# Optimization experiments

Hardware: AMD Instinct MI355X
Metric: run time of the kernel (lower is better)

The kernel has to match this reference:

```python
import jax, jax.numpy as jnp
import numpy as np

G, P, DEG = 1024, 75, 8            # graphs, nodes per graph, out-degree
N, E = G * P, G * P * DEG
KS, DIM = 5, 2
K = KS ** DIM                      # 25 spline weight matrices
VOX = 4                            # 2x2 voxel grid per graph (size=14 over [0,27.99])


def setup_inputs():
    key = jax.random.key(0)
    ks = jax.random.split(key, 14)
    x = jax.random.uniform(ks[0], (N, 1), dtype=jnp.float32)            # pixel intensities
    src = jnp.repeat(jnp.arange(N, dtype=jnp.int32), DEG)
    dst = (src // P) * P + jax.random.randint(ks[1], (E,), 0, P, dtype=jnp.int32)
    edge_index = jnp.stack([src, dst])                                   # [2,E], within-graph edges
    edge_attr = jax.random.uniform(ks[2], (E, DIM), dtype=jnp.float32)  # Cartesian pseudo-coords in [0,1]
    batch = jnp.repeat(jnp.arange(G, dtype=jnp.int32), P)
    pos = jax.random.uniform(ks[3], (N, DIM), dtype=jnp.float32) * 27.99

    def nrm(k, shape, fan_in):
        return jax.random.normal(k, shape, jnp.float32) / np.float32(np.sqrt(fan_in))

    W1 = nrm(ks[4], (K, 1, 32), 1.0)
    root1 = nrm(ks[5], (1, 32), 1.0)
    b1 = jnp.zeros((32,), jnp.float32)
    W2 = nrm(ks[6], (K, 32, 64), 32.0)
    root2 = nrm(ks[7], (32, 64), 32.0)
    b2 = jnp.zeros((64,), jnp.float32)
    W3 = nrm(ks[8], (K, 64, 64), 64.0)
    root3 = nrm(ks[9], (64, 64), 64.0)
    b3 = jnp.zeros((64,), jnp.float32)
    fc1_w = nrm(ks[10], (4 * 64, 128), 256.0)
    fc1_b = jnp.zeros((128,), jnp.float32)
    fc2_w = nrm(ks[11], (128, 10), 128.0)
    fc2_b = jnp.zeros((10,), jnp.float32)
    return dict(x=x, edge_index=edge_index, edge_attr=edge_attr, batch=batch, pos=pos,
                W1=W1, root1=root1, b1=b1, W2=W2, root2=root2, b2=b2,
                W3=W3, root3=root3, b3=b3,
                fc1_w=fc1_w, fc1_b=fc1_b, fc2_w=fc2_w, fc2_b=fc2_b)


def spline_basis(u):
    """Degree-1 open B-spline basis, dim=2, kernel_size=5. u:[E,2] in [0,1].
    Returns basis [E,4] and flat weight indices [E,4]."""
    p = u * (KS - 1)
    lo = jnp.clip(jnp.floor(p), 0.0, KS - 1)
    frac = p - lo
    lo_i = lo.astype(jnp.int32)
    hi_i = jnp.minimum(lo_i + 1, KS - 1)
    w0 = jnp.stack([1.0 - frac[:, 0], frac[:, 0]], 1)   # [E,2]
    w1 = jnp.stack([1.0 - frac[:, 1], frac[:, 1]], 1)
    i0 = jnp.stack([lo_i[:, 0], hi_i[:, 0]], 1)
    i1 = jnp.stack([lo_i[:, 1], hi_i[:, 1]], 1)
    basis = (w0[:, :, None] * w1[:, None, :]).reshape(-1, 4)      # [E,4]
    idx = (i0[:, :, None] + KS * i1[:, None, :]).reshape(-1, 4)   # [E,4]
    return basis, idx


def spline_conv(h, src, dst, basis, idx, W, root, bias):
    # per-node transform under all K kernel weights: [N,K,O]
    y = jnp.einsum('ni,kio->nko', h, W)
    O = W.shape[2]
    msg = jnp.zeros((src.shape[0], O), h.dtype)
    for s in range(4):  # 4 B-spline corner contributions (fixed small loop)
        msg = msg + basis[:, s:s + 1] * y[src, idx[:, s]]
    agg = jax.ops.segment_sum(msg, dst, num_segments=N)
    deg = jax.ops.segment_sum(jnp.ones((src.shape[0],), h.dtype), dst, num_segments=N)
    agg = agg / jnp.maximum(deg, 1.0)[:, None]          # aggr='mean'
    return agg + h @ root + bias


def reference(x, edge_index, edge_attr, batch, pos,
              W1, root1, b1, W2, root2, b2, W3, root3, b3,
              fc1_w, fc1_b, fc2_w, fc2_b):
    src, dst = edge_index[0], edge_index[1]
    basis, idx = spline_basis(edge_attr)
    h = jax.nn.elu(spline_conv(x, src, dst, basis, idx, W1, root1, b1))
    h = jax.nn.elu(spline_conv(h, src, dst, basis, idx, W2, root2, b2))
    h = jax.nn.elu(spline_conv(h, src, dst, basis, idx, W3, root3, b3))
    # voxel_grid(size=14, start=0, end=27.99) -> 2x2 grid per graph
    vox = jnp.clip((pos / 14.0).astype(jnp.int32), 0, 1)          # [N,2]
    cluster = batch * VOX + vox[:, 0] + 2 * vox[:, 1]
    pooled = jax.ops.segment_max(h, cluster, num_segments=G * VOX)
    pooled = jnp.where(jnp.isneginf(pooled), 0.0, pooled)         # empty voxels -> 0
    graph_x = pooled.reshape(G, VOX * 64)                          # [G, 256]
    graph_x = jax.nn.elu(graph_x @ fc1_w + fc1_b)                  # dropout: eval mode (identity)
    logits = graph_x @ fc2_w + fc2_b
    return jax.nn.log_softmax(logits, axis=1)
```

## Files before the change

### kernel.cpp

```cpp
#include <hip/hip_runtime.h>
#include <math.h>

#define NG 1024
#define NP 75
#define NE_G 600
#define E_TOT 614400
#define NK 25
#define NSEG 1875
#define SST 104
#define YTST 104
#define HST 72

typedef _Float16 half8 __attribute__((ext_vector_type(8)));
typedef float floatx4 __attribute__((ext_vector_type(4)));

#define WS_WT2 0
#define WS_WT3 51200
#define WS_R2T 153600
#define WS_R3T 155648

__device__ __forceinline__ float elu_f(float x) {
    return x > 0.f ? x : (expf(x) - 1.f);
}
__device__ __forceinline__ float h16f(unsigned short b) {
    union { unsigned short u; _Float16 h; } c; c.u = b; return (float)c.h;
}
__device__ __forceinline__ _Float16 bits16(unsigned short b) {
    union { unsigned short u; _Float16 h; } c; c.u = b; return c.h;
}
__device__ __forceinline__ unsigned short f16bits(float v) {
    union { _Float16 h; unsigned short u; } c; c.h = (_Float16)v; return c.u;
}

__global__ void __launch_bounds__(256) prep_weights(
    const float* __restrict__ W2, const float* __restrict__ root2,
    const float* __restrict__ W3, const float* __restrict__ root3,
    _Float16* __restrict__ ws)
{
    int i = blockIdx.x * 256 + threadIdx.x;
    int stride = gridDim.x * 256;
    for (int t = i; t < 25 * 64 * 32; t += stride) {
        int k = t >> 11, o = (t >> 5) & 63, ci = t & 31;
        ws[WS_WT2 + t] = (_Float16)W2[(k * 32 + ci) * 64 + o];
    }
    for (int t = i; t < 25 * 64 * 64; t += stride) {
        int k = t >> 12, o = (t >> 6) & 63, ci = t & 63;
        ws[WS_WT3 + t] = (_Float16)W3[(k * 64 + ci) * 64 + o];
    }
    for (int t = i; t < 64 * 32; t += stride) {
        int o = t >> 5, ci = t & 31;
        ws[WS_R2T + t] = (_Float16)root2[ci * 64 + o];
    }
    for (int t = i; t < 64 * 64; t += stride) {
        int o = t >> 6, ci = t & 63;
        ws[WS_R3T + t] = (_Float16)root3[ci * 64 + o];
    }
}

struct EdgeB { int dl; int kk[4]; unsigned short bas[4]; };
__device__ __forceinline__ EdgeB edge_basis(const float* __restrict__ attr,
                                            const int* __restrict__ eidx,
                                            int g, int e) {
    EdgeB r;
    int ge = g * NE_G + e;
    r.dl = eidx[E_TOT + ge] - g * NP;
    float p0 = attr[2 * ge + 0] * 4.f, p1 = attr[2 * ge + 1] * 4.f;
    float fl0 = fminf(fmaxf(floorf(p0), 0.f), 4.f);
    float fl1 = fminf(fmaxf(floorf(p1), 0.f), 4.f);
    float fr0 = p0 - fl0, fr1 = p1 - fl1;
    int i00 = (int)fl0, i10 = (int)fl1;
    int i01 = min(i00 + 1, 4), i11 = min(i10 + 1, 4);
    float w0a[2] = {1.f - fr0, fr0};
    float w1a[2] = {1.f - fr1, fr1};
    int i0a[2] = {i00, i01};
    int i1a[2] = {i10, i11};
    #pragma unroll
    for (int a = 0; a < 2; ++a)
        #pragma unroll
        for (int b = 0; b < 2; ++b) {
            int s = a * 2 + b;
            r.kk[s] = i0a[a] + 5 * i1a[b];
            r.bas[s] = f16bits(w0a[a] * w1a[b]);
        }
    return r;
}

template<int CIN>
__device__ __forceinline__ void conv_layer(
    const _Float16* __restrict__ Wt,
    const _Float16* __restrict__ rootT,
    const float* __restrict__ bias,
    _Float16* __restrict__ sb_S,
    _Float16* __restrict__ sb_yT,
    _Float16* __restrict__ sb_h,
    const unsigned* __restrict__ sb_list,
    const int* __restrict__ sb_koff,
    const float* __restrict__ sb_rdeg,
    int tid, int lane, int wid)
{
    const int m = lane & 15, q = (lane >> 4) & 3;
    const int o0 = wid * 16, o = o0 + m;
    constexpr int KK = CIN / 32;

    half8 Ah[5][KK];
    #pragma unroll
    for (int mt = 0; mt < 5; ++mt)
        #pragma unroll
        for (int kk = 0; kk < KK; ++kk)
            Ah[mt][kk] = *(const half8*)&sb_h[(mt * 16 + m) * HST + kk * 32 + q * 8];

    floatx4 agg[5];
    #pragma unroll
    for (int mt = 0; mt < 5; ++mt) agg[mt] = (floatx4){0.f, 0.f, 0.f, 0.f};

    half8 Bc[KK], Bn[KK];
    #pragma unroll
    for (int kk = 0; kk < KK; ++kk)
        Bc[kk] = *(const half8*)&Wt[(0 * 64 + o) * CIN + kk * 32 + q * 8];

    for (int k = 0; k < NK; ++k) {
        const int jb = sb_koff[k] + tid, kend = sb_koff[k + 1];
        unsigned upre = (jb < kend) ? sb_list[jb] : 0u;
        const _Float16* nb = (k < NK - 1) ? &Wt[((k + 1) * 64 + o) * CIN]
                                          : &rootT[o * CIN];
        #pragma unroll
        for (int kk = 0; kk < KK; ++kk)
            Bn[kk] = *(const half8*)&nb[kk * 32 + q * 8];
        for (int t = tid; t < 80 * SST / 8; t += 256)
            ((floatx4*)sb_S)[t] = (floatx4){0.f, 0.f, 0.f, 0.f};
        #pragma unroll
        for (int mt = 0; mt < 5; ++mt) {
            floatx4 c = {0.f, 0.f, 0.f, 0.f};
            #pragma unroll
            for (int kk = 0; kk < KK; ++kk)
                c = __builtin_amdgcn_mfma_f32_16x16x32_f16(Ah[mt][kk], Bc[kk], c, 0, 0, 0);
            #pragma unroll
            for (int r = 0; r < 4; ++r) {
                int n = mt * 16 + q * 4 + r;
                sb_yT[o * YTST + n] = (_Float16)c[r];
            }
        }
        __syncthreads();
        {
            bool first = true;
            for (int j = jb; j < kend; j += 256) {
                unsigned u = first ? upre : sb_list[j];
                first = false;
                if (u >> 16)
                    sb_S[((u >> 7) & 127) * SST + (u & 127)] = bits16((unsigned short)(u >> 16));
            }
        }
        __syncthreads();
        {
            half8 B0 = *(const half8*)&sb_yT[o * YTST + 0 + q * 8];
            half8 B1 = *(const half8*)&sb_yT[o * YTST + 32 + q * 8];
            half8 B2 = *(const half8*)&sb_yT[o * YTST + 64 + q * 8];
            #pragma unroll
            for (int mt = 0; mt < 5; ++mt) {
                half8 a0 = *(const half8*)&sb_S[(mt * 16 + m) * SST + 0 + q * 8];
                half8 a1 = *(const half8*)&sb_S[(mt * 16 + m) * SST + 32 + q * 8];
                half8 a2 = *(const half8*)&sb_S[(mt * 16 + m) * SST + 64 + q * 8];
                floatx4 c = agg[mt];
                c = __builtin_amdgcn_mfma_f32_16x16x32_f16(a0, B0, c, 0, 0, 0);
                c = __builtin_amdgcn_mfma_f32_16x16x32_f16(a1, B1, c, 0, 0, 0);
                c = __builtin_amdgcn_mfma_f32_16x16x32_f16(a2, B2, c, 0, 0, 0);
                agg[mt] = c;
            }
        }
        #pragma unroll
        for (int kk = 0; kk < KK; ++kk) Bc[kk] = Bn[kk];
        __syncthreads();
    }

    float bo = bias[o];
    #pragma unroll
    for (int mt = 0; mt < 5; ++mt) {
        floatx4 c = {0.f, 0.f, 0.f, 0.f};
        #pragma unroll
        for (int kk = 0; kk < KK; ++kk)
            c = __builtin_amdgcn_mfma_f32_16x16x32_f16(Ah[mt][kk], Bc[kk], c, 0, 0, 0);
        #pragma unroll
        for (int r = 0; r < 4; ++r) {
            int n = mt * 16 + q * 4 + r;
            if (n < NP) {
                float v = agg[mt][r] * sb_rdeg[n] + c[r] + bo;
                sb_h[n * HST + o] = (_Float16)elu_f(v);
            }
        }
    }
    __syncthreads();
}

__global__ void __launch_bounds__(256, 3) mnist_spline_fused(
    const float* __restrict__ xg,
    const int* __restrict__ eidx,
    const float* __restrict__ attr,
    const float* __restrict__ pos,
    const float* __restrict__ W1, const float* __restrict__ root1, const float* __restrict__ b1,
    const float* __restrict__ b2, const float* __restrict__ b3,
    const float* __restrict__ fc1w, const float* __restrict__ fc1b,
    const float* __restrict__ fc2w, const float* __restrict__ fc2b,
    const _Float16* __restrict__ ws,
    float* __restrict__ out)
{
    const int g = blockIdx.x;
    const int tid = threadIdx.x;
    const int lane = tid & 63;
    const int wid = tid >> 6;

    __shared__ __align__(16) _Float16 sb_S[80 * SST];
    __shared__ __align__(16) _Float16 sb_yT[64 * YTST];
    __shared__ __align__(16) _Float16 sb_h[80 * HST];
    __shared__ __align__(16) unsigned sb_list[NE_G * 4];
    __shared__ int sb_koff[26];
    __shared__ float sb_x[80];
    __shared__ float sb_rdeg[80];
    __shared__ int sb_deg[80];
    __shared__ unsigned sb_vmask[12];
    __shared__ unsigned sb_wsum[8];

    unsigned* cnt32 = (unsigned*)sb_S;
    unsigned short* segoff = (unsigned short*)((char*)sb_S + 7552);
    _Float16* T1 = sb_S;
    _Float16* W1T = (_Float16*)((char*)sb_S + 11312);
    float* fc_part = (float*)sb_S;
    float* fc_gx = (float*)((char*)sb_S + 2048);
    float* fc_z1 = (float*)((char*)sb_S + 3072);

    for (int p = tid; p < 80; p += 256) sb_deg[p] = 0;
    for (int p = tid; p < NSEG; p += 256) cnt32[p] = 0u;
    for (int p = tid; p < 5 * HST / 2; p += 256)
        ((unsigned*)&sb_h[NP * HST])[p] = 0u;
    for (int p = tid; p < 64 * 12; p += 256) {
        int ch = p / 12, c = p % 12;
        ((unsigned*)sb_yT)[ch * (YTST / 2) + 40 + c] = 0u;
    }
    if (tid < 12) sb_vmask[tid] = 0u;
    for (int p = tid; p < 32 * 32; p += 256) {
        int k = p >> 5, o = p & 31;
        W1T[o * 32 + k] = (k < NK) ? (_Float16)W1[k * 32 + o] : (_Float16)0.f;
    }
    __syncthreads();

    for (int e = tid; e < NE_G; e += 256) {
        EdgeB eb = edge_basis(attr, eidx, g, e);
        atomicAdd(&sb_deg[eb.dl], 1);
        #pragma unroll
        for (int s = 0; s < 4; ++s)
            atomicAdd(&cnt32[eb.kk[s] * NP + eb.dl], 1u);
    }
    for (int n = tid; n < NP; n += 256) {
        int gn = g * NP + n;
        sb_x[n] = xg[gn];
        int v0 = min(max((int)(pos[2 * gn] * (1.f / 14.f)), 0), 1);
        int v1 = min(max((int)(pos[2 * gn + 1] * (1.f / 14.f)), 0), 1);
        int v = v0 + 2 * v1;
        atomicOr(&sb_vmask[v * 3 + (n >> 5)], 1u << (n & 31));
    }
    __syncthreads();

    {
        int base = tid * 8;
        unsigned c8[8], lsum = 0;
        #pragma unroll
        for (int i = 0; i < 8; ++i) {
            int idx = base + i;
            c8[i] = (idx < NSEG) ? cnt32[idx] : 0u;
            lsum += c8[i];
        }
        unsigned v = lsum;
        #pragma unroll
        for (int d = 1; d < 64; d <<= 1) {
            unsigned ov = __shfl_up(v, d);
            if (lane >= d) v += ov;
        }
        if (lane == 63) sb_wsum[wid] = v;
        __syncthreads();
        unsigned wpre = 0;
        for (int w2 = 0; w2 < wid; ++w2) wpre += sb_wsum[w2];
        unsigned run = wpre + v - lsum;
        #pragma unroll
        for (int i = 0; i < 8; ++i) {
            int idx = base + i;
            if (idx < NSEG + 1) segoff[idx] = (unsigned short)run;
            if (idx < NSEG) cnt32[idx] = run;
            run += c8[i];
        }
        if (tid < 80) sb_rdeg[tid] = (tid < NP) ? 1.f / fmaxf((float)sb_deg[tid], 1.f) : 0.f;
    }
    __syncthreads();

    for (int e = tid; e < NE_G; e += 256) {
        EdgeB eb = edge_basis(attr, eidx, g, e);
        int srcl = e >> 3;
        #pragma unroll
        for (int s = 0; s < 4; ++s) {
            unsigned p = atomicAdd(&cnt32[eb.kk[s] * NP + eb.dl], 1u);
            sb_list[p] = ((unsigned)eb.bas[s] << 16) | ((unsigned)eb.dl << 7) | (unsigned)srcl;
        }
    }
    if (tid < 26) sb_koff[tid] = segoff[min(tid * NP, NSEG)];
    __syncthreads();

    for (int s = tid; s < NSEG; s += 256) {
        int s0 = segoff[s], s1 = segoff[s + 1];
        float tsum = 0.f;
        for (int j = s0; j < s1; ++j) {
            unsigned u = sb_list[j];
            if (!(u >> 16)) continue;
            int src = u & 127;
            float bsum = h16f((unsigned short)(u >> 16));
            for (int j2 = j + 1; j2 < s1; ++j2) {
                unsigned u2 = sb_list[j2];
                if ((u2 & 127) == (unsigned)src && (u2 >> 16)) {
                    bsum += h16f((unsigned short)(u2 >> 16));
                    sb_list[j2] = u2 & 0xFFFFu;
                }
            }
            sb_list[j] = ((unsigned)f16bits(bsum) << 16) | (u & 0xFFFFu);
            tsum += bsum * sb_x[src];
        }
        int k = s / NP, d = s - k * NP;
        T1[d * 40 + k] = (_Float16)tsum;
    }
    for (int t = tid; t < NP * 15 + 5 * 40; t += 256) {
        int d, k;
        if (t < NP * 15) { d = t / 15; k = NK + t % 15; }
        else { int t2 = t - NP * 15; d = NP + t2 / 40; k = t2 % 40; }
        T1[d * 40 + k] = (_Float16)0.f;
    }
    __syncthreads();

    if (wid < 2) {
        const int m = lane & 15, q = (lane >> 4) & 3;
        const int o = wid * 16 + m;
        half8 Bw = *(const half8*)&W1T[o * 32 + q * 8];
        float rt = root1[o], bo = b1[o];
        #pragma unroll
        for (int mt = 0; mt < 5; ++mt) {
            half8 a = *(const half8*)&T1[(mt * 16 + m) * 40 + q * 8];
            floatx4 c = {0.f, 0.f, 0.f, 0.f};
            c = __builtin_amdgcn_mfma_f32_16x16x32_f16(a, Bw, c, 0, 0, 0);
            #pragma unroll
            for (int r = 0; r < 4; ++r) {
                int n = mt * 16 + q * 4 + r;
                if (n < NP) {
                    float v = c[r] * sb_rdeg[n] + sb_x[n] * rt + bo;
                    sb_h[n * HST + o] = (_Float16)elu_f(v);
                }
            }
        }
    }
    __syncthreads();

    conv_layer<32>(ws + WS_WT2, ws + WS_R2T, b2, sb_S, sb_yT, sb_h,
                   sb_list, sb_koff, sb_rdeg, tid, lane, wid);
    conv_layer<64>(ws + WS_WT3, ws + WS_R3T, b3, sb_S, sb_yT, sb_h,
                   sb_list, sb_koff, sb_rdeg, tid, lane, wid);

    {
        int v = wid, o = lane;
        float mval = -INFINITY;
        #pragma unroll 25
        for (int n = 0; n < NP; ++n) {
            float val = (float)sb_h[n * HST + o];
            bool sel = (sb_vmask[v * 3 + (n >> 5)] >> (n & 31)) & 1;
            mval = sel ? fmaxf(mval, val) : mval;
        }
        fc_gx[v * 64 + o] = (mval == -INFINITY) ? 0.f : mval;
    }
    __syncthreads();

    {
        float acc0 = 0.f, acc1 = 0.f;
        #pragma unroll 8
        for (int i = 0; i < 64; ++i) {
            int ii = wid * 64 + i;
            float xv = fc_gx[ii];
            acc0 += xv * fc1w[ii * 128 + lane];
            acc1 += xv * fc1w[ii * 128 + 64 + lane];
        }
        fc_part[wid * 128 + lane] = acc0;
        fc_part[wid * 128 + 64 + lane] = acc1;
    }
    __syncthreads();
    if (tid < 128) {
        float v = fc_part[tid] + fc_part[128 + tid] + fc_part[256 + tid] + fc_part[384 + tid]
                + fc1b[tid];
        fc_z1[tid] = elu_f(v);
    }
    __syncthreads();

    if (wid == 0) {
        int o = lane & 15, sg = lane >> 4;
        float acc = 0.f;
        if (o < 10) {
            #pragma unroll 8
            for (int i = sg * 32; i < sg * 32 + 32; ++i)
                acc += fc_z1[i] * fc2w[i * 10 + o];
        }
        acc += __shfl_xor(acc, 16);
        acc += __shfl_xor(acc, 32);
        float logit = (o < 10) ? (acc + fc2b[o]) : 0.f;
        float lv = (o < 10) ? logit : -INFINITY;
        float mx = lv;
        #pragma unroll
        for (int d = 1; d < 16; d <<= 1) mx = fmaxf(mx, __shfl_xor(mx, d));
        float ex = (o < 10) ? expf(logit - mx) : 0.f;
        float se = ex;
        #pragma unroll
        for (int d = 1; d < 16; d <<= 1) se += __shfl_xor(se, d);
        if (lane < 10) out[g * 10 + lane] = logit - mx - logf(se);
    }
}

extern "C" void kernel_launch(void* const* d_in, const int* in_sizes, int n_in,
                              void* d_out, int out_size, void* d_ws, size_t ws_size,
                              hipStream_t stream) {
    const float* xg    = (const float*)d_in[0];
    const int*   eidx  = (const int*)d_in[1];
    const float* attr  = (const float*)d_in[2];
    const float* pos   = (const float*)d_in[4];
    const float* W1    = (const float*)d_in[5];
    const float* root1 = (const float*)d_in[6];
    const float* b1    = (const float*)d_in[7];
    const float* W2    = (const float*)d_in[8];
    const float* root2 = (const float*)d_in[9];
    const float* b2    = (const float*)d_in[10];
    const float* W3    = (const float*)d_in[11];
    const float* root3 = (const float*)d_in[12];
    const float* b3    = (const float*)d_in[13];
    const float* fc1w  = (const float*)d_in[14];
    const float* fc1b  = (const float*)d_in[15];
    const float* fc2w  = (const float*)d_in[16];
    const float* fc2b  = (const float*)d_in[17];
    float* out = (float*)d_out;
    _Float16* ws = (_Float16*)d_ws;

    prep_weights<<<160, 256, 0, stream>>>(W2, root2, W3, root3, ws);
    mnist_spline_fused<<<NG, 256, 0, stream>>>(
        xg, eidx, attr, pos, W1, root1, b1, b2, b3,
        fc1w, fc1b, fc2w, fc2b, ws, out);
}
```

Measured before the change: 264.2 us.

## Merge S-matrix clear and scatter per destination row, drop one barrier per k

New measurement: 299.6 us. 13.4% more time.

```diff
diff --git a/kernel.cpp b/kernel.cpp
--- a/kernel.cpp
+++ b/kernel.cpp
@@ -7,8 +7,8 @@
 #define E_TOT 614400
 #define NK 25
 #define NSEG 1875
-#define SST 104
-#define YTST 104
+#define SST 80
+#define YTST 80
 #define HST 72
 
 typedef _Float16 half8 __attribute__((ext_vector_type(8)));
@@ -94,12 +94,12 @@
     _Float16* __restrict__ sb_yT,
     _Float16* __restrict__ sb_h,
     const unsigned* __restrict__ sb_list,
-    const int* __restrict__ sb_koff,
+    const unsigned short* __restrict__ sb_segoff,
     const float* __restrict__ sb_rdeg,
     int tid, int lane, int wid)
 {
     const int m = lane & 15, q = (lane >> 4) & 3;
-    const int o0 = wid * 16, o = o0 + m;
+    const int o = wid * 16 + m;
     constexpr int KK = CIN / 32;
 
     half8 Ah[5][KK];
@@ -115,51 +115,62 @@
 
     half8 Bc[KK], Bn[KK];
     #pragma unroll
-    for (int kk = 0; kk < KK; ++kk)
+    for (int kk = 0; kk < KK; ++kk) {
         Bc[kk] = *(const half8*)&Wt[(0 * 64 + o) * CIN + kk * 32 + q * 8];
+        Bn[kk] = *(const half8*)&Wt[(1 * 64 + o) * CIN + kk * 32 + q * 8];
+    }
+
+    const int sd = tid / 3, sc = tid % 3;
+    const bool sact = (tid < 225);
+    floatx4* zp = (floatx4*)&sb_S[sd * SST + sc * 32];
+    const int znum = (sc < 2) ? 4 : 2;
+
+    const half8 zero8 = {};
 
     for (int k = 0; k < NK; ++k) {
-        const int jb = sb_koff[k] + tid, kend = sb_koff[k + 1];
-        unsigned upre = (jb < kend) ? sb_list[jb] : 0u;
-        const _Float16* nb = (k < NK - 1) ? &Wt[((k + 1) * 64 + o) * CIN]
-                                          : &rootT[o * CIN];
-        #pragma unroll
-        for (int kk = 0; kk < KK; ++kk)
-            Bn[kk] = *(const half8*)&nb[kk * 32 + q * 8];
-        for (int t = tid; t < 80 * SST / 8; t += 256)
-            ((floatx4*)sb_S)[t] = (floatx4){0.f, 0.f, 0.f, 0.f};
+        if (sact) {
+            #pragma unroll 4
+            for (int z = 0; z < znum; ++z) zp[z] = (floatx4){0.f, 0.f, 0.f, 0.f};
+            int j0 = sb_segoff[k * NP + sd], j1 = sb_segoff[k * NP + sd + 1];
+            for (int j = j0; j < j1; ++j) {
+                unsigned u = sb_list[j];
+                int src = u & 127;
+                if ((src >> 5) == sc && (u >> 16))
+                    sb_S[sd * SST + src] = bits16((unsigned short)(u >> 16));
+            }
+        }
         #pragma unroll
         for (int mt = 0; mt < 5; ++mt) {
             floatx4 c = {0.f, 0.f, 0.f, 0.f};
             #pragma unroll
             for (int kk = 0; kk < KK; ++kk)
                 c = __builtin_amdgcn_mfma_f32_16x16x32_f16(Ah[mt][kk], Bc[kk], c, 0, 0, 0);
+            union { _Float16 h[4]; unsigned long long u64; } p;
+            p.h[0] = (_Float16)c[0]; p.h[1] = (_Float16)c[1];
+            p.h[2] = (_Float16)c[2]; p.h[3] = (_Float16)c[3];
+            *(unsigned long long*)&sb_yT[o * YTST + mt * 16 + q * 4] = p.u64;
+        }
+        #pragma unroll
+        for (int kk = 0; kk < KK; ++kk) Bc[kk] = Bn[kk];
+        if (k < NK - 1) {
+            const _Float16* nb = (k + 2 < NK) ? &Wt[((k + 2) * 64 + o) * CIN]
+                                              : &rootT[o * CIN];
             #pragma unroll
-            for (int r = 0; r < 4; ++r) {
-                int n = mt * 16 + q * 4 + r;
-                sb_yT[o * YTST + n] = (_Float16)c[r];
-            }
-        }
-        __syncthreads();
-        {
-            bool first = true;
-            for (int j = jb; j < kend; j += 256) {
-                unsigned u = first ? upre : sb_list[j];
-                first = false;
-                if (u >> 16)
-                    sb_S[((u >> 7) & 127) * SST + (u & 127)] = bits16((unsigned short)(u >> 16));
-            }
+            for (int kk = 0; kk < KK; ++kk)
+                Bn[kk] = *(const half8*)&nb[kk * 32 + q * 8];
         }
         __syncthreads();
         {
             half8 B0 = *(const half8*)&sb_yT[o * YTST + 0 + q * 8];
             half8 B1 = *(const half8*)&sb_yT[o * YTST + 32 + q * 8];
-            half8 B2 = *(const half8*)&sb_yT[o * YTST + 64 + q * 8];
+            half8 B2 = zero8;
+            if (q < 2) B2 = *(const half8*)&sb_yT[o * YTST + 64 + q * 8];
             #pragma unroll
             for (int mt = 0; mt < 5; ++mt) {
                 half8 a0 = *(const half8*)&sb_S[(mt * 16 + m) * SST + 0 + q * 8];
                 half8 a1 = *(const half8*)&sb_S[(mt * 16 + m) * SST + 32 + q * 8];
-                half8 a2 = *(const half8*)&sb_S[(mt * 16 + m) * SST + 64 + q * 8];
+                half8 a2 = zero8;
+                if (q < 2) a2 = *(const half8*)&sb_S[(mt * 16 + m) * SST + 64 + q * 8];
                 floatx4 c = agg[mt];
                 c = __builtin_amdgcn_mfma_f32_16x16x32_f16(a0, B0, c, 0, 0, 0);
                 c = __builtin_amdgcn_mfma_f32_16x16x32_f16(a1, B1, c, 0, 0, 0);
@@ -167,8 +178,6 @@
                 agg[mt] = c;
             }
         }
-        #pragma unroll
-        for (int kk = 0; kk < KK; ++kk) Bc[kk] = Bn[kk];
         __syncthreads();
     }
 
@@ -212,7 +221,7 @@
     __shared__ __align__(16) _Float16 sb_yT[64 * YTST];
     __shared__ __align__(16) _Float16 sb_h[80 * HST];
     __shared__ __align__(16) unsigned sb_list[NE_G * 4];
-    __shared__ int sb_koff[26];
+    __shared__ __align__(16) unsigned short sb_segoff[NSEG + 1];
     __shared__ float sb_x[80];
     __shared__ float sb_rdeg[80];
     __shared__ int sb_deg[80];
@@ -220,9 +229,8 @@
     __shared__ unsigned sb_wsum[8];
 
     unsigned* cnt32 = (unsigned*)sb_S;
-    unsigned short* segoff = (unsigned short*)((char*)sb_S + 7552);
     _Float16* T1 = sb_S;
-    _Float16* W1T = (_Float16*)((char*)sb_S + 11312);
+    _Float16* W1T = sb_yT;
     float* fc_part = (float*)sb_S;
     float* fc_gx = (float*)((char*)sb_S + 2048);
     float* fc_z1 = (float*)((char*)sb_S + 3072);
@@ -231,10 +239,8 @@
     for (int p = tid; p < NSEG; p += 256) cnt32[p] = 0u;
     for (int p = tid; p < 5 * HST / 2; p += 256)
         ((unsigned*)&sb_h[NP * HST])[p] = 0u;
-    for (int p = tid; p < 64 * 12; p += 256) {
-        int ch = p / 12, c = p % 12;
-        ((unsigned*)sb_yT)[ch * (YTST / 2) + 40 + c] = 0u;
-    }
+    for (int p = tid; p < 5 * SST / 2; p += 256)
+        ((unsigned*)&sb_S[NP * SST])[p] = 0u;
     if (tid < 12) sb_vmask[tid] = 0u;
     for (int p = tid; p < 32 * 32; p += 256) {
         int k = p >> 5, o = p & 31;
@@ -279,12 +285,17 @@
         unsigned wpre = 0;
         for (int w2 = 0; w2 < wid; ++w2) wpre += sb_wsum[w2];
         unsigned run = wpre + v - lsum;
+        unsigned short so[8];
+        #pragma unroll
+        for (int i = 0; i < 8; ++i) {
+            so[i] = (unsigned short)run;
+            run += c8[i];
+        }
         #pragma unroll
         for (int i = 0; i < 8; ++i) {
             int idx = base + i;
-            if (idx < NSEG + 1) segoff[idx] = (unsigned short)run;
-            if (idx < NSEG) cnt32[idx] = run;
-            run += c8[i];
+            if (idx < NSEG + 1) sb_segoff[idx] = so[i];
+            if (idx < NSEG) cnt32[idx] = so[i];
         }
         if (tid < 80) sb_rdeg[tid] = (tid < NP) ? 1.f / fmaxf((float)sb_deg[tid], 1.f) : 0.f;
     }
@@ -299,11 +310,10 @@
             sb_list[p] = ((unsigned)eb.bas[s] << 16) | ((unsigned)eb.dl << 7) | (unsigned)srcl;
         }
     }
-    if (tid < 26) sb_koff[tid] = segoff[min(tid * NP, NSEG)];
     __syncthreads();
 
     for (int s = tid; s < NSEG; s += 256) {
-        int s0 = segoff[s], s1 = segoff[s + 1];
+        int s0 = sb_segoff[s], s1 = sb_segoff[s + 1];
         float tsum = 0.f;
         for (int j = s0; j < s1; ++j) {
             unsigned u = sb_list[j];
@@ -354,9 +364,9 @@
     __syncthreads();
 
     conv_layer<32>(ws + WS_WT2, ws + WS_R2T, b2, sb_S, sb_yT, sb_h,
-                   sb_list, sb_koff, sb_rdeg, tid, lane, wid);
+                   sb_list, sb_segoff, sb_rdeg, tid, lane, wid);
     conv_layer<64>(ws + WS_WT3, ws + WS_R3T, b3, sb_S, sb_yT, sb_h,
-                   sb_list, sb_koff, sb_rdeg, tid, lane, wid);
+                   sb_list, sb_segoff, sb_rdeg, tid, lane, wid);
 
     {
         int v = wid, o = lane;
```
